# Optimization experiments

Hardware: AMD Instinct MI355X
Metric: run time of the kernel (lower is better)

The kernel has to match this reference:

```python
import jax, jax.numpy as jnp
import numpy as np

N_NODES = 50000
N_EDGES = 800000
IN_NF = 64
OUT_NF = 64
HID = 128
H = 4
D = 64
HD = H * D
EDGE_IN = 2 * IN_NF + 1 + 6   # 135
MSG_IN = HID + 1 + 3 + 6      # 138


def _p(key, i, shape, scale=0.02):
    return scale * jax.random.normal(jax.random.fold_in(key, i), shape, dtype=jnp.float32)


def setup_inputs() -> dict:
    key = jax.random.key(0)
    ks = jax.random.split(key, 4)
    inp = {
        "h": jax.random.normal(ks[0], (N_NODES, IN_NF), dtype=jnp.float32),
        "x": jax.random.normal(ks[1], (N_NODES, 3), dtype=jnp.float32),
        "edge_index": jax.random.randint(ks[2], (2, N_EDGES), 0, N_NODES, dtype=jnp.int32),
        "mask": jnp.ones((N_EDGES,), dtype=bool),
    }
    pk = jax.random.fold_in(key, 7)
    i = iter(range(100))
    inp.update({
        "Wq": _p(pk, next(i), (IN_NF, HD)), "bq": jnp.zeros((HD,)),
        "Wk": _p(pk, next(i), (IN_NF, HD)), "bk": jnp.zeros((HD,)),
        "Wv": _p(pk, next(i), (IN_NF, HD)), "bv": jnp.zeros((HD,)),
        "Wo": _p(pk, next(i), (HD, OUT_NF)), "bo": jnp.zeros((OUT_NF,)),
        "pw1": _p(pk, next(i), (1, HID // 2)), "pb1": jnp.zeros((HID // 2,)),
        "pw2": _p(pk, next(i), (HID // 2, H)), "pb2": jnp.zeros((H,)),
        "ew1": _p(pk, next(i), (EDGE_IN, HID)), "eb1": jnp.zeros((HID,)),
        "ew2": _p(pk, next(i), (HID, HID)), "eb2": jnp.zeros((HID,)),
        "eww": _p(pk, next(i), (HID, H)), "ewb": jnp.zeros((H,)),
        "mw1": _p(pk, next(i), (MSG_IN, HID)), "mb1": jnp.zeros((HID,)),
        "mw2": _p(pk, next(i), (HID, HID)), "mb2": jnp.zeros((HID,)),
        "gw": _p(pk, next(i), (HID, H)), "gb": jnp.zeros((H,)),
        "cw1": _p(pk, next(i), (HID, HID)), "cb1": jnp.zeros((HID,)),
        "cw2": _p(pk, next(i), (HID, H)), "cb2": jnp.zeros((H,)),
        "coord_weights": jnp.ones((H,)),
        "xw1": _p(pk, next(i), (HID, HID)), "xb1": jnp.zeros((HID,)),
        "xw2": _p(pk, next(i), (HID, H)), "xb2": jnp.zeros((H,)),
    })
    return inp


def reference(h, x, edge_index, mask,
              Wq, bq, Wk, bk, Wv, bv, Wo, bo,
              pw1, pb1, pw2, pb2,
              ew1, eb1, ew2, eb2, eww, ewb,
              mw1, mb1, mw2, mb2,
              gw, gb, cw1, cb1, cw2, cb2,
              coord_weights, xw1, xb1, xw2, xb2):
    silu = jax.nn.silu
    row, col = edge_index[0], edge_index[1]
    n = h.shape[0]

    q = (h @ Wq + bq).reshape(n, H, D)
    k = (h @ Wk + bk).reshape(n, H, D)
    v = (h @ Wv + bv).reshape(n, H, D)

    rel_pos = x[row] - x[col]                         # [E,3]
    rel_dist = jnp.sum(rel_pos ** 2, -1, keepdims=True)  # [E,1]
    pos_enc = silu(rel_dist @ pw1 + pb1) @ pw2 + pb2     # [E,H]

    # torch .std() is unbiased (ddof=1)
    xn = (x - x.mean(0, keepdims=True)) / (jnp.std(x, 0, keepdims=True, ddof=1) + 1e-8)

    edge_attr = jnp.concatenate([h[row], h[col], rel_dist, xn[row], xn[col]], -1)
    ef = silu(edge_attr @ ew1 + eb1) @ ew2 + eb2      # [E,HID]
    ewt = ef @ eww + ewb                              # [E,H]

    attn = jnp.einsum('ehd,ehd->eh', q[row], k[col]) / jnp.sqrt(jnp.float32(D))
    attn = attn + pos_enc + ewt
    attn = jnp.where(mask[:, None], attn, jnp.float32(-1e9))

    amax = jax.ops.segment_max(attn, row, num_segments=n)   # [N,H]
    attn = jnp.exp(attn - amax[row])
    asum = jax.ops.segment_sum(attn, row, num_segments=n)
    attn = attn / (asum[row] + 1e-8)                         # [E,H]

    msg_in = jnp.concatenate([ef, attn.mean(1, keepdims=True), rel_pos, xn[row], xn[col]], -1)
    msgs = silu(msg_in @ mw1 + mb1) @ mw2 + mb2              # [E,HID]

    gates = jax.nn.sigmoid(msgs @ gw + gb)                   # [E,H]
    cwts = silu(msgs @ cw1 + cb1) @ cw2 + cb2                # [E,H]

    # per-head index_add into the same buffer == sum over heads of the scalar weight
    s = jnp.sum(gates * cwts * coord_weights, -1, keepdims=True)  # [E,1]
    base = 0.9 * rel_pos + 0.1 * x[col]
    coord_update = jax.ops.segment_sum(s * base / (n - 1), row, num_segments=n)

    cross_v = jnp.cross(rel_pos, jnp.roll(rel_pos, 1, axis=0))
    cg = silu(msgs @ xw1 + xb1) @ xw2 + xb2                  # [E,H]
    cross_s = jnp.sum(cg, -1, keepdims=True)
    coord_update = coord_update + jax.ops.segment_sum(cross_s * cross_v / (n - 1), row, num_segments=n)

    wv = jax.ops.segment_sum(attn[..., None] * v[col], row, num_segments=n)  # [N,H,D]
    out = wv.reshape(n, HD) @ Wo + bo
    return out, coord_update
```

## Files before the change

kernel.cpp:

```cpp
#include <hip/hip_runtime.h>
#include <hip/hip_bf16.h>

#define NN 50000
#define NE 800000

typedef __bf16 bf16x8 __attribute__((ext_vector_type(8)));
typedef float f4v __attribute__((ext_vector_type(4)));

__device__ __forceinline__ float silu_f(float v){
  return v*__builtin_amdgcn_rcpf(1.0f+__expf(-v));
}
__device__ __forceinline__ float bf2f(unsigned int u){ return __uint_as_float(u<<16); }
__device__ __forceinline__ unsigned bfr(float f){
  unsigned b = __float_as_uint(f);
  return b + 0x7fffu + ((b>>16)&1u);
}
__device__ __forceinline__ unsigned short f2bf(float f){ return (unsigned short)(bfr(f)>>16); }
__device__ __forceinline__ unsigned pk2(float a, float b){
  unsigned r;
  asm("v_cvt_pk_bf16_f32 %0, %1, %2" : "=v"(r) : "v"(a), "v"(b));
  return r;
}

union U8 { unsigned short us[8]; uint4 u4; };

__device__ __forceinline__ void pack8(unsigned short* dst, float4 a, float4 b){
  uint4 u;
  u.x = pk2(a.x,a.y); u.y = pk2(a.z,a.w);
  u.z = pk2(b.x,b.y); u.w = pk2(b.z,b.w);
  *(uint4*)dst = u;
}

__device__ __forceinline__ int lidx(int e, int c, int CH){
  return (e*CH + ((c & ~7) | ((c ^ e) & 7))) << 3;
}

template<int KC, int CH>
__device__ __forceinline__ void gemm_rm(const unsigned short* act, const unsigned short* wf,
                                        int wu, int lane, f4v (&acc)[4][2]){
  int le = lane & 15, quad = lane >> 4;
  #pragma unroll
  for (int kc=0;kc<KC;kc++){
    bf16x8 a0 = *(const bf16x8*)(wf + (((wu*2  )*KC + kc)<<9) + lane*8);
    bf16x8 a1 = *(const bf16x8*)(wf + (((wu*2+1)*KC + kc)<<9) + lane*8);
    int chunk = kc*4 + quad;
    #pragma unroll
    for (int et=0;et<4;et++){
      bf16x8 b = *(const bf16x8*)(act + lidx(et*16+le, chunk, CH));
      acc[et][0] = __builtin_amdgcn_mfma_f32_16x16x32_bf16(a0, b, acc[et][0], 0,0,0);
      acc[et][1] = __builtin_amdgcn_mfma_f32_16x16x32_bf16(a1, b, acc[et][1], 0,0,0);
    }
  }
}

template<int CH, bool SILU, bool BIAS>
__device__ __forceinline__ void epi_rm(unsigned short* dst, const f4v (&acc)[4][2],
                                       const float* bias, int wu, int lane){
  int le = lane & 15, quad = lane >> 4;
  #pragma unroll
  for (int ot=0; ot<2; ot++){
    float4 bv = make_float4(0,0,0,0);
    if (BIAS) bv = *(const float4*)(bias + wu*32 + ot*16 + quad*4);
    int chunk = wu*4 + ot*2 + (quad>>1);
    int soff = (quad&1)*4;
    #pragma unroll
    for (int et=0; et<4; et++){
      float v0=acc[et][ot][0], v1=acc[et][ot][1], v2=acc[et][ot][2], v3=acc[et][ot][3];
      if (BIAS){ v0+=bv.x; v1+=bv.y; v2+=bv.z; v3+=bv.w; }
      if (SILU){ v0=silu_f(v0); v1=silu_f(v1); v2=silu_f(v2); v3=silu_f(v3); }
      uint2 u; u.x = pk2(v0,v1); u.y = pk2(v2,v3);
      *(uint2*)(dst + lidx(et*16+le, chunk, CH) + soff) = u;
    }
  }
}

template<int CH>
__device__ __forceinline__ void mfma_head(const unsigned short* buf, const unsigned short* whf,
                                          int wu, int lane, float* dst ){
  int le = lane & 15, quad = lane >> 4;
  f4v hacc = {0.f,0.f,0.f,0.f};
  #pragma unroll
  for (int kc=0;kc<4;kc++){
    bf16x8 a = *(const bf16x8*)(whf + (kc<<9) + lane*8);
    bf16x8 b = *(const bf16x8*)(buf + lidx(wu*16+le, kc*4+quad, CH));
    hacc = __builtin_amdgcn_mfma_f32_16x16x32_bf16(a, b, hacc, 0,0,0);
  }
  if (quad==0){
    #pragma unroll
    for (int r=0;r<4;r++) dst[r*65 + wu*16 + le] = hacc[r];
  }
}

__global__ __launch_bounds__(256) void k_zero(float* __restrict__ p, int n){
  int i = blockIdx.x*256 + threadIdx.x;
  if (i < n) p[i] = 0.f;
}

__global__ __launch_bounds__(256) void k_wcomb(const float* __restrict__ ew2, const float* __restrict__ eww,
                                               const float* __restrict__ eb2, const float* __restrict__ ewb,
                                               const float* __restrict__ pb2,
                                               float* __restrict__ wcomb, float* __restrict__ stats){
  int t = threadIdx.x;
  #pragma unroll
  for (int o=t;o<512;o+=256){
    int i=o>>2, hh=o&3;
    float s=0.f;
    for (int j=0;j<128;j++) s += ew2[i*128+j]*eww[j*4+hh];
    wcomb[o]=s;
  }
  if (t<4){
    float s=0.f;
    for (int j=0;j<128;j++) s += eb2[j]*eww[j*4+t];
    stats[12+t] = s + ewb[t] + pb2[t];
  }
}

__global__ __launch_bounds__(256) void k_wfold(const float* __restrict__ A, const float* __restrict__ Bm,
                                               const float* __restrict__ abias, const float* __restrict__ b2,
                                               float* __restrict__ dstW, float* __restrict__ dstB){
  int idx = blockIdx.x*256 + threadIdx.x;
  if (idx >= 129*128) return;
  int i = idx>>7, n = idx&127;
  if (i<128){
    float s=0.f;
    for (int j=0;j<128;j++) s += A[i*128+j]*Bm[j*128+n];
    dstW[i*128+n]=s;
  } else {
    float s=b2[n];
    for (int j=0;j<128;j++) s += abias[j]*Bm[j*128+n];
    dstB[n]=s;
  }
}

__global__ __launch_bounds__(256) void k_wfoldm(const float* __restrict__ ew2, const float* __restrict__ mw1,
                                                const float* __restrict__ eb2, const float* __restrict__ mb1,
                                                float* __restrict__ dstW, float* __restrict__ dstB){
  int idx = blockIdx.x*256 + threadIdx.x;
  if (idx >= 139*128) return;
  int i = idx>>7, n = idx&127;
  if (i<128){
    float s=0.f;
    for (int j=0;j<128;j++) s += ew2[i*128+j]*mw1[j*128+n];
    dstW[i*128+n]=s;
  } else if (i<138){
    dstW[i*128+n] = mw1[i*128+n];
  } else {
    float s=mb1[n];
    for (int j=0;j<128;j++) s += eb2[j]*mw1[j*128+n];
    dstB[n]=s;
  }
}

__global__ __launch_bounds__(256) void k_wfoldg(const float* __restrict__ mw2, const float* __restrict__ gw,
                                                const float* __restrict__ mb2, const float* __restrict__ gb,
                                                float* __restrict__ dstW, float* __restrict__ dstB){
  int idx = blockIdx.x*256 + threadIdx.x;
  if (idx >= 129*4) return;
  int i = idx>>2, hh = idx&3;
  if (i<128){
    float s=0.f;
    for (int j=0;j<128;j++) s += mw2[i*128+j]*gw[j*4+hh];
    dstW[i*4+hh]=s;
  } else {
    float s=gb[hh];
    for (int j=0;j<128;j++) s += mb2[j]*gw[j*4+hh];
    dstB[hh]=s;
  }
}

__global__ __launch_bounds__(256) void k_wprep(const float* __restrict__ src, unsigned short* __restrict__ dst,
                                               int Kreal, int KC){
  int idx = blockIdx.x*256 + threadIdx.x;
  int tot = 8*KC*512;
  if (idx >= tot) return;
  int nt  = idx/(KC*512); int rem = idx%(KC*512);
  int kc  = rem>>9;       int r2  = rem&511;
  int lq  = r2>>3;        int j   = r2&7;
  int k   = kc*32 + (lq>>4)*8 + j;
  int n   = nt*16 + (lq&15);
  float v = (k < Kreal) ? src[k*128 + n] : 0.f;
  dst[idx] = f2bf(v);
}

__global__ __launch_bounds__(256) void k_wprepq(const float* __restrict__ src, unsigned short* __restrict__ dst){
  int idx = blockIdx.x*256 + threadIdx.x;
  if (idx >= 16384) return;
  int nt  = idx>>10;  int rem = idx&1023;
  int kc  = rem>>9;   int r2  = rem&511;
  int lq  = r2>>3;    int j   = r2&7;
  int k   = kc*32 + (lq>>4)*8 + j;
  int n   = nt*16 + (lq&15);
  dst[idx] = f2bf(src[k*256 + n]);
}

__global__ __launch_bounds__(256) void k_wprep4(const float* __restrict__ src, unsigned short* __restrict__ dst){
  int idx = blockIdx.x*256 + threadIdx.x;
  if (idx >= 2048) return;
  int kc = idx>>9; int r2 = idx&511; int lq = r2>>3; int j = r2&7;
  int k = kc*32 + (lq>>4)*8 + j;
  int n = lq&15;
  dst[idx] = f2bf((n<4) ? src[k*4+n] : 0.f);
}

__global__ __launch_bounds__(256) void k_stats(const float* __restrict__ x, float* __restrict__ stats){
  int i = blockIdx.x*256 + threadIdx.x;
  float v0=0.f,v1=0.f,v2=0.f;
  if (i < NN){ v0=x[i*3+0]; v1=x[i*3+1]; v2=x[i*3+2]; }
  float vals[6] = {v0,v1,v2,v0*v0,v1*v1,v2*v2};
  __shared__ float red[256];
  for (int c=0;c<6;c++){
    red[threadIdx.x]=vals[c];
    __syncthreads();
    for (int off=128; off>0; off>>=1){
      if (threadIdx.x < off) red[threadIdx.x] += red[threadIdx.x+off];
      __syncthreads();
    }
    if (threadIdx.x==0) atomicAdd(&stats[c], red[0]);
    __syncthreads();
  }
}

__global__ __launch_bounds__(64) void k_statsfin(float* __restrict__ stats){
  int t = threadIdx.x;
  if (t < 3){
    float s = stats[t], sq = stats[3+t];
    float mean = s/(float)NN;
    float var = (sq - s*s/(float)NN)/(float)(NN-1);
    float sd = sqrtf(var);
    stats[6+t] = mean;
    stats[9+t] = 1.0f/(sd + 1e-8f);
  }
}

__global__ __launch_bounds__(256) void k_qkv2(const float* __restrict__ h,
    const unsigned short* __restrict__ wqf,
    const float* __restrict__ bq, const float* __restrict__ bk, const float* __restrict__ bv,
    unsigned short* __restrict__ q, unsigned short* __restrict__ kk, unsigned short* __restrict__ v){
  __shared__ __align__(16) unsigned short hstage[64*8*8];
  int t = threadIdx.x; int lane = t & 63; int w = t >> 6;
  int wu = __builtin_amdgcn_readfirstlane(w);
  int r0 = blockIdx.x*64;
  {
    int row = r0 + lane;
    float4 a = make_float4(0,0,0,0), b2 = make_float4(0,0,0,0),
           c = make_float4(0,0,0,0), d2 = make_float4(0,0,0,0);
    if (row < NN){
      const float* hr = h + (size_t)row*64 + wu*16;
      a  = *(const float4*)(hr);    b2 = *(const float4*)(hr+4);
      c  = *(const float4*)(hr+8);  d2 = *(const float4*)(hr+12);
    }
    pack8(&hstage[lidx(lane, 2*wu,   8)], a, b2);
    pack8(&hstage[lidx(lane, 2*wu+1, 8)], c, d2);
  }
  __syncthreads();
  int le = lane & 15, quad = lane >> 4;
  #pragma unroll
  for (int ti=0; ti<12; ti++){
    int tt = ti*4 + wu;
    f4v acc[4];
    f4v z = {0.f,0.f,0.f,0.f};
    acc[0]=z; acc[1]=z; acc[2]=z; acc[3]=z;
    #pragma unroll
    for (int kc=0;kc<2;kc++){
      bf16x8 a = *(const bf16x8*)(wqf + ((tt*2 + kc)<<9) + lane*8);
      int chunk = kc*4 + quad;
      #pragma unroll
      for (int et=0;et<4;et++){
        bf16x8 b = *(const bf16x8*)(hstage + lidx(et*16+le, chunk, 8));
        acc[et] = __builtin_amdgcn_mfma_f32_16x16x32_bf16(a, b, acc[et], 0,0,0);
      }
    }
    int mat = tt>>4; int ct = tt&15;
    const float* bias = (mat==0)? bq : (mat==1)? bk : bv;
    unsigned short* outp = (mat==0)? q : (mat==1)? kk : v;
    float4 bv4 = *(const float4*)(bias + ct*16 + quad*4);
    int col = ct*16 + quad*4;
    #pragma unroll
    for (int et=0;et<4;et++){
      int row2 = r0 + et*16 + le;
      if (row2 < NN){
        float v0=acc[et][0]+bv4.x, v1=acc[et][1]+bv4.y, v2=acc[et][2]+bv4.z, v3=acc[et][3]+bv4.w;
        if (mat<2){
          uint2 u; u.x = pk2(v0,v1); u.y = pk2(v2,v3);
          *(uint2*)(outp + (size_t)row2*256 + col) = u;
        } else {
          int head = col>>6, dd = col&63;
          unsigned short* vp = outp + (size_t)row2*256 + (size_t)dd*4 + head;
          vp[0]  = f2bf(v0);
          vp[4]  = f2bf(v1);
          vp[8]  = f2bf(v2);
          vp[12] = f2bf(v3);
        }
      }
    }
  }
}

__global__ __launch_bounds__(256) void k_count(const int* __restrict__ ei, int* __restrict__ counts){
  int e = blockIdx.x*256 + threadIdx.x;
  if (e < NE) atomicAdd(&counts[ei[e]], 1);
}

__global__ __launch_bounds__(256) void k_scan(int* __restrict__ counts, int* __restrict__ offs){
  __shared__ int ps[256];
  int t = threadIdx.x;
  int base = t*196;
  int s = 0;
  for (int i=0;i<196;i++){ int idx = base+i; if (idx < NN) s += counts[idx]; }
  ps[t]=s; __syncthreads();
  for (int off=1; off<256; off<<=1){
    int vv = (t>=off)? ps[t-off] : 0;
    __syncthreads();
    ps[t]+=vv;
    __syncthreads();
  }
  int run = ps[t]-s;
  for (int i=0;i<196;i++){
    int idx = base+i;
    if (idx < NN){ int c = counts[idx]; offs[idx]=run; counts[idx]=run; run+=c; }
  }
  if (t==255) offs[NN]=run;
}

__global__ __launch_bounds__(256) void k_fill(const int* __restrict__ ei, int* __restrict__ cursor, int* __restrict__ elist){
  int e = blockIdx.x*256 + threadIdx.x;
  if (e < NE){
    int r = ei[e];
    int p = atomicAdd(&cursor[r],1);
    elist[p] = e;
  }
}

__global__ __launch_bounds__(256) void k_e1(
    const float* __restrict__ h, const float* __restrict__ x, const int* __restrict__ ei,
    const float* __restrict__ stats,
    const unsigned short* __restrict__ qb, const unsigned short* __restrict__ kb,
    const unsigned short* __restrict__ wfrag, const unsigned short* __restrict__ whfrag,
    const float* __restrict__ eb1,
    const float* __restrict__ pw1, const float* __restrict__ pb1,
    const float* __restrict__ pw2,
    float* __restrict__ asum, float* __restrict__ eattn){
  __shared__ __align__(16) unsigned short bufIn[64*24*8];
  __shared__ float logit_s[256];
  __shared__ float ewt2_s[4*65];
  __shared__ float pos_s[4*65];
  __shared__ float rd_s[64], xnr_s[192], xnc_s[192];
  __shared__ int row_s[64], col_s[64];
  int t = threadIdx.x; int lane = t & 63; int w = t >> 6;
  int wu = __builtin_amdgcn_readfirstlane(w);
  int ebase = blockIdx.x * 64;

  for (int i=t;i<260;i+=256) pos_s[i]=0.f;
  if (t < 64){
    int ge = ebase + t;
    int r = ei[ge], c = ei[NE+ge];
    row_s[t]=r; col_s[t]=c;
    float xr0=x[r*3],xr1=x[r*3+1],xr2=x[r*3+2];
    float xc0=x[c*3],xc1=x[c*3+1],xc2=x[c*3+2];
    float rp0=xr0-xc0, rp1=xr1-xc1, rp2=xr2-xc2;
    rd_s[t]=rp0*rp0+rp1*rp1+rp2*rp2;
    float m0=stats[6],m1=stats[7],m2=stats[8],s0=stats[9],s1=stats[10],s2=stats[11];
    xnr_s[t*3+0]=(xr0-m0)*s0; xnr_s[t*3+1]=(xr1-m1)*s1; xnr_s[t*3+2]=(xr2-m2)*s2;
    xnc_s[t*3+0]=(xc0-m0)*s0; xnc_s[t*3+1]=(xc1-m1)*s1; xnc_s[t*3+2]=(xc2-m2)*s2;
  }
  __syncthreads();

  for (int ii=0; ii<16; ii++){
    int e = wu*16+ii;
    int r = row_s[e], c = col_s[e];
    uint2 qu = *(const uint2*)(qb + (size_t)r*256 + lane*4);
    uint2 ku = *(const uint2*)(kb + (size_t)c*256 + lane*4);
    float d = bf2f(qu.x&0xffffu)*bf2f(ku.x&0xffffu)
            + bf2f(qu.x>>16)   *bf2f(ku.x>>16)
            + bf2f(qu.y&0xffffu)*bf2f(ku.y&0xffffu)
            + bf2f(qu.y>>16)   *bf2f(ku.y>>16);
    d += __shfl_xor(d,1,16); d += __shfl_xor(d,2,16);
    d += __shfl_xor(d,4,16); d += __shfl_xor(d,8,16);
    if ((lane&15)==0) logit_s[e*4 + (lane>>4)] = d*0.125f;
  }
  {
    int jb = wu*16;
    float rd = rd_s[lane];
    float p0=0,p1=0,p2=0,p3=0;
    for (int j=jb; j<jb+16; j++){
      float hp = rd*pw1[j] + pb1[j];
      float hs = silu_f(hp);
      const float4 w4 = *(const float4*)(pw2 + j*4);
      p0+=hs*w4.x; p1+=hs*w4.y; p2+=hs*w4.z; p3+=hs*w4.w;
    }
    atomicAdd(&pos_s[0*65+lane],p0);
    atomicAdd(&pos_s[1*65+lane],p1);
    atomicAdd(&pos_s[2*65+lane],p2);
    atomicAdd(&pos_s[3*65+lane],p3);
  }
  {
    const float* hr = h + (size_t)row_s[lane]*64 + wu*16;
    pack8(&bufIn[lidx(lane, 2*wu,   24)], *(const float4*)(hr),   *(const float4*)(hr+4));
    pack8(&bufIn[lidx(lane, 2*wu+1, 24)], *(const float4*)(hr+8), *(const float4*)(hr+12));
    const float* hc = h + (size_t)col_s[lane]*64 + wu*16;
    pack8(&bufIn[lidx(lane, 8+2*wu, 24)], *(const float4*)(hc),   *(const float4*)(hc+4));
    pack8(&bufIn[lidx(lane, 9+2*wu, 24)], *(const float4*)(hc+8), *(const float4*)(hc+12));
  }
  if (t < 64){
    pack8(&bufIn[lidx(t,16,24)],
          make_float4(rd_s[t], xnr_s[t*3+0], xnr_s[t*3+1], xnr_s[t*3+2]),
          make_float4(xnc_s[t*3+0], xnc_s[t*3+1], xnc_s[t*3+2], 0.f));
  }
  {
    uint4 z4 = make_uint4(0,0,0,0);
    int e = t&63, j = t>>6;
    if (j < 3) *(uint4*)&bufIn[lidx(e, 17+j, 24)] = z4;
  }
  __syncthreads();
  f4v acc[4][2];
  f4v z = {0.f,0.f,0.f,0.f};
  #pragma unroll
  for (int et=0;et<4;et++){ acc[et][0]=z; acc[et][1]=z; }
  gemm_rm<5,24>(bufIn, wfrag + 0, wu, lane, acc);
  __syncthreads();
  epi_rm<24,true,true>(bufIn, acc, eb1, wu, lane);
  __syncthreads();
  mfma_head<24>(bufIn, whfrag + 0, wu, lane, ewt2_s);
  __syncthreads();
  {
    int e2 = t>>2, hh = t&3;
    float lg = logit_s[t] + stats[12+hh] + ewt2_s[hh*65+e2] + pos_s[hh*65+e2];
    float ex = __expf(lg);
    eattn[(size_t)ebase*4 + t] = ex;
    atomicAdd(&asum[row_s[e2]*4 + hh], ex);
  }
}

__global__ __launch_bounds__(256) void k_e2(
    const float* __restrict__ h, const float* __restrict__ x, const int* __restrict__ ei,
    const float* __restrict__ stats,
    const float* __restrict__ asum, const float* __restrict__ eattn,
    const unsigned short* __restrict__ wfrag, const unsigned short* __restrict__ whfrag,
    const float* __restrict__ eb1, const float* __restrict__ fbias,
    const float* __restrict__ cb2, const float* __restrict__ coordw,
    const float* __restrict__ xb2,
    float* __restrict__ cvec){
  __shared__ __align__(16) unsigned short bufIn[64*24*8];
  __shared__ float am_s[64];
  __shared__ float g_s[4*65], c_s[4*65], xx_s[4*65];
  __shared__ float s_s[64], cs_s[64];
  __shared__ float rp_s[192], rd_s[64], xnr_s[192], xnc_s[192], xc_s[192];
  __shared__ int row_s[64], col_s[64];
  int t = threadIdx.x; int lane = t & 63; int w = t >> 6;
  int wu = __builtin_amdgcn_readfirstlane(w);
  int ebase = blockIdx.x * 64;

  if (t < 64){
    int ge = ebase + t;
    int r = ei[ge], c = ei[NE+ge];
    row_s[t]=r; col_s[t]=c;
    float xr0=x[r*3],xr1=x[r*3+1],xr2=x[r*3+2];
    float xc0=x[c*3],xc1=x[c*3+1],xc2=x[c*3+2];
    float rp0=xr0-xc0, rp1=xr1-xc1, rp2=xr2-xc2;
    rp_s[t*3+0]=rp0; rp_s[t*3+1]=rp1; rp_s[t*3+2]=rp2;
    rd_s[t]=rp0*rp0+rp1*rp1+rp2*rp2;
    xc_s[t*3+0]=xc0; xc_s[t*3+1]=xc1; xc_s[t*3+2]=xc2;
    float m0=stats[6],m1=stats[7],m2=stats[8],s0=stats[9],s1=stats[10],s2=stats[11];
    xnr_s[t*3+0]=(xr0-m0)*s0; xnr_s[t*3+1]=(xr1-m1)*s1; xnr_s[t*3+2]=(xr2-m2)*s2;
    xnc_s[t*3+0]=(xc0-m0)*s0; xnc_s[t*3+1]=(xc1-m1)*s1; xnc_s[t*3+2]=(xc2-m2)*s2;
  }
  __syncthreads();
  {
    int e2 = t>>2; int hh = t&3;
    float ex = eattn[(size_t)ebase*4 + t];
    float a = ex / (asum[row_s[e2]*4 + hh] + 1e-8f);
    a += __shfl_xor(a,1); a += __shfl_xor(a,2);
    if (hh==0) am_s[e2] = 0.25f*a;
  }
  {
    const float* hr = h + (size_t)row_s[lane]*64 + wu*16;
    pack8(&bufIn[lidx(lane, 2*wu,   24)], *(const float4*)(hr),   *(const float4*)(hr+4));
    pack8(&bufIn[lidx(lane, 2*wu+1, 24)], *(const float4*)(hr+8), *(const float4*)(hr+12));
    const float* hc = h + (size_t)col_s[lane]*64 + wu*16;
    pack8(&bufIn[lidx(lane, 8+2*wu, 24)], *(const float4*)(hc),   *(const float4*)(hc+4));
    pack8(&bufIn[lidx(lane, 9+2*wu, 24)], *(const float4*)(hc+8), *(const float4*)(hc+12));
  }
  if (t < 64){
    pack8(&bufIn[lidx(t,16,24)],
          make_float4(rd_s[t], xnr_s[t*3+0], xnr_s[t*3+1], xnr_s[t*3+2]),
          make_float4(xnc_s[t*3+0], xnc_s[t*3+1], xnc_s[t*3+2], 0.f));
  }
  {
    uint4 z4 = make_uint4(0,0,0,0);
    int e = t&63, j = t>>6;
    if (j < 3) *(uint4*)&bufIn[lidx(e, 17+j, 24)] = z4;
  }
  __syncthreads();
  f4v acc[4][2];
  f4v z = {0.f,0.f,0.f,0.f};
  #pragma unroll
  for (int et=0;et<4;et++){ acc[et][0]=z; acc[et][1]=z; }
  gemm_rm<5,24>(bufIn, wfrag + 0, wu, lane, acc);
  __syncthreads();
  epi_rm<24,true,true>(bufIn, acc, eb1, wu, lane);
  if (t < 64){
    pack8(&bufIn[lidx(t,16,24)],
          make_float4(am_s[t], rp_s[t*3+0], rp_s[t*3+1], rp_s[t*3+2]),
          make_float4(xnr_s[t*3+0], xnr_s[t*3+1], xnr_s[t*3+2], xnc_s[t*3+0]));
    pack8(&bufIn[lidx(t,17,24)],
          make_float4(xnc_s[t*3+1], xnc_s[t*3+2], 0.f, 0.f),
          make_float4(0.f,0.f,0.f,0.f));
  }
  __syncthreads();
  #pragma unroll
  for (int et=0;et<4;et++){ acc[et][0]=z; acc[et][1]=z; }
  gemm_rm<5,24>(bufIn, wfrag + 20480, wu, lane, acc);
  __syncthreads();
  epi_rm<24,true,true>(bufIn, acc, fbias + 0, wu, lane);
  __syncthreads();
  mfma_head<24>(bufIn, whfrag + 2048, wu, lane, g_s);
  f4v ax[4][2];
  #pragma unroll
  for (int et=0;et<4;et++){ acc[et][0]=z; acc[et][1]=z; ax[et][0]=z; ax[et][1]=z; }
  {
    const unsigned short* wfc = wfrag + 40960;
    const unsigned short* wfx = wfrag + 57344;
    int le = lane&15, quad = lane>>4;
    #pragma unroll
    for (int kc=0;kc<4;kc++){
      bf16x8 ac0 = *(const bf16x8*)(wfc + (((wu*2  )*4 + kc)<<9) + lane*8);
      bf16x8 ac1 = *(const bf16x8*)(wfc + (((wu*2+1)*4 + kc)<<9) + lane*8);
      bf16x8 ax0 = *(const bf16x8*)(wfx + (((wu*2  )*4 + kc)<<9) + lane*8);
      bf16x8 ax1 = *(const bf16x8*)(wfx + (((wu*2+1)*4 + kc)<<9) + lane*8);
      int chunk = kc*4 + quad;
      #pragma unroll
      for (int et=0;et<4;et++){
        bf16x8 b = *(const bf16x8*)(bufIn + lidx(et*16+le, chunk, 24));
        acc[et][0] = __builtin_amdgcn_mfma_f32_16x16x32_bf16(ac0, b, acc[et][0], 0,0,0);
        acc[et][1] = __builtin_amdgcn_mfma_f32_16x16x32_bf16(ac1, b, acc[et][1], 0,0,0);
        ax[et][0]  = __builtin_amdgcn_mfma_f32_16x16x32_bf16(ax0, b, ax[et][0], 0,0,0);
        ax[et][1]  = __builtin_amdgcn_mfma_f32_16x16x32_bf16(ax1, b, ax[et][1], 0,0,0);
      }
    }
  }
  __syncthreads();
  epi_rm<24,true,true>(bufIn, acc, fbias + 128, wu, lane);
  __syncthreads();
  mfma_head<24>(bufIn, whfrag + 4096, wu, lane, c_s);
  __syncthreads();
  epi_rm<24,true,true>(bufIn, ax, fbias + 256, wu, lane);
  __syncthreads();
  mfma_head<24>(bufIn, whfrag + 6144, wu, lane, xx_s);
  __syncthreads();
  {
    int e2 = t>>2; int hh = t&3;
    float g = __builtin_amdgcn_rcpf(1.0f+__expf(-(g_s[hh*65+e2]+fbias[384+hh])));
    float cwv = c_s[hh*65+e2]+cb2[hh];
    float sv = g*cwv*coordw[hh];
    float csv = xx_s[hh*65+e2]+xb2[hh];
    sv += __shfl_xor(sv,1);  sv += __shfl_xor(sv,2);
    csv += __shfl_xor(csv,1); csv += __shfl_xor(csv,2);
    if (hh==0){ s_s[e2]=sv; cs_s[e2]=csv; }
  }
  __syncthreads();
  if (t < 64){
    int ge = ebase + t;
    float rp0=rp_s[t*3],rp1=rp_s[t*3+1],rp2=rp_s[t*3+2];
    float pp0,pp1,pp2;
    if (t > 0){ pp0=rp_s[(t-1)*3]; pp1=rp_s[(t-1)*3+1]; pp2=rp_s[(t-1)*3+2]; }
    else {
      int gp = (ebase==0)? (NE-1) : (ebase-1);
      int rr=ei[gp], cc2=ei[NE+gp];
      pp0=x[rr*3]-x[cc2*3]; pp1=x[rr*3+1]-x[cc2*3+1]; pp2=x[rr*3+2]-x[cc2*3+2];
    }
    float cv0 = rp1*pp2 - rp2*pp1;
    float cv1 = rp2*pp0 - rp0*pp2;
    float cv2 = rp0*pp1 - rp1*pp0;
    float sv = s_s[t], csv = cs_s[t];
    const float inv = 1.0f/49999.0f;
    cvec[(size_t)ge*3+0] = (sv*(0.9f*rp0+0.1f*xc_s[t*3+0]) + csv*cv0)*inv;
    cvec[(size_t)ge*3+1] = (sv*(0.9f*rp1+0.1f*xc_s[t*3+1]) + csv*cv1)*inv;
    cvec[(size_t)ge*3+2] = (sv*(0.9f*rp2+0.1f*xc_s[t*3+2]) + csv*cv2)*inv;
  }
}

__global__ __launch_bounds__(256) void k_aggout(
    const int* __restrict__ ei, const int* __restrict__ offs, const int* __restrict__ elist,
    const float* __restrict__ eattn, const unsigned short* __restrict__ vb,
    const float* __restrict__ cvec, const float* __restrict__ Wo, const float* __restrict__ bo,
    const float* __restrict__ asum,
    float* __restrict__ outp){
  __shared__ float wvs[4*256];
  int t = threadIdx.x; int lane = t & 63; int w = t >> 6;
  int node = blockIdx.x*4 + w;
  const int* colp = ei + NE;
  int s0 = offs[node], s1 = offs[node+1];
  float a0=0,a1=0,a2=0,a3=0,cc=0;
  int i = s0;
  for (; i+4<=s1; i+=4){
    int e0=elist[i], e1=elist[i+1], e2=elist[i+2], e3=elist[i+3];
    int c0=colp[e0], c1=colp[e1], c2=colp[e2], c3=colp[e3];
    uint2 v0 = *(const uint2*)(vb + (size_t)c0*256 + lane*4);
    uint2 v1 = *(const uint2*)(vb + (size_t)c1*256 + lane*4);
    uint2 v2 = *(const uint2*)(vb + (size_t)c2*256 + lane*4);
    uint2 v3 = *(const uint2*)(vb + (size_t)c3*256 + lane*4);
    float4 at0 = *(const float4*)(eattn + (size_t)e0*4);
    float4 at1 = *(const float4*)(eattn + (size_t)e1*4);
    float4 at2 = *(const float4*)(eattn + (size_t)e2*4);
    float4 at3 = *(const float4*)(eattn + (size_t)e3*4);
    if (lane < 3) cc += cvec[(size_t)e0*3+lane] + cvec[(size_t)e1*3+lane]
                      + cvec[(size_t)e2*3+lane] + cvec[(size_t)e3*3+lane];
    a0 += at0.x*bf2f(v0.x&0xffffu) + at1.x*bf2f(v1.x&0xffffu) + at2.x*bf2f(v2.x&0xffffu) + at3.x*bf2f(v3.x&0xffffu);
    a1 += at0.y*bf2f(v0.x>>16)     + at1.y*bf2f(v1.x>>16)     + at2.y*bf2f(v2.x>>16)     + at3.y*bf2f(v3.x>>16);
    a2 += at0.z*bf2f(v0.y&0xffffu) + at1.z*bf2f(v1.y&0xffffu) + at2.z*bf2f(v2.y&0xffffu) + at3.z*bf2f(v3.y&0xffffu);
    a3 += at0.w*bf2f(v0.y>>16)     + at1.w*bf2f(v1.y>>16)     + at2.w*bf2f(v2.y>>16)     + at3.w*bf2f(v3.y>>16);
  }
  for (; i<s1; i++){
    int e0 = elist[i];
    int c0 = colp[e0];
    uint2 v0 = *(const uint2*)(vb + (size_t)c0*256 + lane*4);
    float4 at0 = *(const float4*)(eattn + (size_t)e0*4);
    if (lane < 3) cc += cvec[(size_t)e0*3+lane];
    a0 += at0.x*bf2f(v0.x&0xffffu);
    a1 += at0.y*bf2f(v0.x>>16);
    a2 += at0.z*bf2f(v0.y&0xffffu);
    a3 += at0.w*bf2f(v0.y>>16);
  }
  {
    const float* as = asum + (size_t)node*4;
    a0 /= (as[0] + 1e-8f);
    a1 /= (as[1] + 1e-8f);
    a2 /= (as[2] + 1e-8f);
    a3 /= (as[3] + 1e-8f);
  }
  wvs[w*256 +       lane]=a0;
  wvs[w*256 +  64 + lane]=a1;
  wvs[w*256 + 128 + lane]=a2;
  wvs[w*256 + 192 + lane]=a3;
  if (lane < 3) outp[(size_t)NN*64 + (size_t)node*3 + lane] = cc;
  float o = bo[lane];
  #pragma unroll 4
  for (int k2=0;k2<256;k2++) o += wvs[w*256+k2] * Wo[k2*64+lane];
  outp[(size_t)node*64 + lane] = o;
}

extern "C" void kernel_launch(void* const* d_in, const int* in_sizes, int n_in,
                              void* d_out, int out_size, void* d_ws, size_t ws_size,
                              hipStream_t stream) {
  const float* h  = (const float*)d_in[0];
  const float* x  = (const float*)d_in[1];
  const int*   ei = (const int*)d_in[2];
  const float* Wq=(const float*)d_in[4];  const float* bq=(const float*)d_in[5];
  const float* Wk=(const float*)d_in[6];  const float* bk=(const float*)d_in[7];
  const float* Wv=(const float*)d_in[8];  const float* bv=(const float*)d_in[9];
  const float* Wo=(const float*)d_in[10]; const float* bo=(const float*)d_in[11];
  const float* pw1=(const float*)d_in[12]; const float* pb1=(const float*)d_in[13];
  const float* pw2=(const float*)d_in[14]; const float* pb2=(const float*)d_in[15];
  const float* ew1=(const float*)d_in[16]; const float* eb1=(const float*)d_in[17];
  const float* ew2=(const float*)d_in[18]; const float* eb2=(const float*)d_in[19];
  const float* eww=(const float*)d_in[20]; const float* ewb=(const float*)d_in[21];
  const float* mw1=(const float*)d_in[22]; const float* mb1=(const float*)d_in[23];
  const float* mw2=(const float*)d_in[24]; const float* mb2=(const float*)d_in[25];
  const float* gw=(const float*)d_in[26];  const float* gb=(const float*)d_in[27];
  const float* cw1=(const float*)d_in[28]; const float* cb1=(const float*)d_in[29];
  const float* cw2=(const float*)d_in[30]; const float* cb2=(const float*)d_in[31];
  const float* coordw=(const float*)d_in[32];
  const float* xw1=(const float*)d_in[33]; const float* xb1=(const float*)d_in[34];
  const float* xw2=(const float*)d_in[35]; const float* xb2=(const float*)d_in[36];

  char* B = (char*)d_ws;
  float* eattn = (float*)(B + 0);
  float* cvec  = (float*)(B + 12800000);
  float* stats = (float*)(B + 22400000);
  float* asum  = (float*)(B + 22400064);
  int* counts  = (int*)(B + 23200064);
  int* offs    = (int*)(B + 23400064);
  unsigned short* wfrag = (unsigned short*)(B + 23600080);
  int* elist   = (int*)(B + 23813088);
  unsigned short* qb = (unsigned short*)(B + 27013088);
  unsigned short* kb = (unsigned short*)(B + 52613088);
  unsigned short* vb = (unsigned short*)(B + 78213088);
  unsigned short* whfrag = (unsigned short*)(B + 103813088);
  float* fbias = (float*)(wfrag + 73728);
  float* wcomb = (float*)elist;
  float* wgf   = wcomb + 512;
  float* wmf   = wgf + 512;
  float* wcf   = wmf + 17664;
  float* wxf   = wcf + 16384;
  unsigned short* qkvf = (unsigned short*)eattn;

  k_zero<<<977,256,0,stream>>>(stats, 250016);
  k_wcomb<<<1,256,0,stream>>>(ew2, eww, eb2, ewb, pb2, wcomb, stats);
  k_wfoldm<<<70,256,0,stream>>>(ew2, mw1, eb2, mb1, wmf, fbias + 0);
  k_wfold<<<65,256,0,stream>>>(mw2, cw1, mb2, cb1, wcf, fbias + 128);
  k_wfold<<<65,256,0,stream>>>(mw2, xw1, mb2, xb1, wxf, fbias + 256);
  k_wfoldg<<<3,256,0,stream>>>(mw2, gw, mb2, gb, wgf, fbias + 384);
  k_wprep<<<80,256,0,stream>>>(ew1, wfrag + 0,     135, 5);
  k_wprep<<<80,256,0,stream>>>(wmf, wfrag + 20480, 138, 5);
  k_wprep<<<64,256,0,stream>>>(wcf, wfrag + 40960, 128, 4);
  k_wprep<<<64,256,0,stream>>>(wxf, wfrag + 57344, 128, 4);
  k_wprepq<<<64,256,0,stream>>>(Wq, qkvf + 0);
  k_wprepq<<<64,256,0,stream>>>(Wk, qkvf + 16384);
  k_wprepq<<<64,256,0,stream>>>(Wv, qkvf + 32768);
  k_wprep4<<<8,256,0,stream>>>(wcomb, whfrag + 0);
  k_wprep4<<<8,256,0,stream>>>(wgf, whfrag + 2048);
  k_wprep4<<<8,256,0,stream>>>(cw2, whfrag + 4096);
  k_wprep4<<<8,256,0,stream>>>(xw2, whfrag + 6144);

  k_stats<<<196,256,0,stream>>>(x, stats);
  k_statsfin<<<1,64,0,stream>>>(stats);
  k_qkv2<<<782,256,0,stream>>>(h, qkvf, bq, bk, bv, qb, kb, vb);
  k_count<<<3125,256,0,stream>>>(ei,counts);
  k_scan<<<1,256,0,stream>>>(counts,offs);
  k_fill<<<3125,256,0,stream>>>(ei,counts,elist);
  k_e1<<<12500,256,0,stream>>>(h,x,ei,stats,qb,kb,wfrag,whfrag,eb1,pw1,pb1,pw2,asum,eattn);
  k_e2<<<12500,256,0,stream>>>(h,x,ei,stats,asum,eattn,wfrag,whfrag,eb1,fbias,cb2,coordw,xb2,cvec);
  k_aggout<<<12500,256,0,stream>>>(ei,offs,elist,eattn,vb,cvec,Wo,bo,asum,(float*)d_out);
}
```

Baseline: 1.313 ms.

## Add second LDS activation buffer in k_e2 to drop barriers between GEMM stages

Adds a separate shared-memory buffer (bufA) for hidden activations so the first GEMM's epilogue can write without waiting for all waves to finish reading the input buffer. The message-side extra features are pre-packed into chunks 18-19 of the input buffer, and the folded message weight is re-laid out (zero-padded to 160 rows) so that its K chunk 4 reads those chunks directly. The coord and cross epilogues and heads now run back-to-back on two buffers, which removes several __syncthreads. The attention-mean computation moves into the per-edge packing thread. The cost is extra LDS per block, which may reduce occupancy.

```diff
diff --git a/kernel.cpp b/kernel.cpp
--- a/kernel.cpp
+++ b/kernel.cpp
@@ -136,14 +136,15 @@
                                                 const float* __restrict__ eb2, const float* __restrict__ mb1,
                                                 float* __restrict__ dstW, float* __restrict__ dstB){
   int idx = blockIdx.x*256 + threadIdx.x;
-  if (idx >= 139*128) return;
+  if (idx >= 161*128) return;
   int i = idx>>7, n = idx&127;
   if (i<128){
     float s=0.f;
     for (int j=0;j<128;j++) s += ew2[i*128+j]*mw1[j*128+n];
     dstW[i*128+n]=s;
-  } else if (i<138){
-    dstW[i*128+n] = mw1[i*128+n];
+  } else if (i<160){
+    int r = i-144;
+    dstW[i*128+n] = (r>=0 && r<10) ? mw1[(128+r)*128+n] : 0.f;
   } else {
     float s=mb1[n];
     for (int j=0;j<128;j++) s += eb2[j]*mw1[j*128+n];
@@ -441,7 +442,7 @@
     const float* __restrict__ xb2,
     float* __restrict__ cvec){
   __shared__ __align__(16) unsigned short bufIn[64*24*8];
-  __shared__ float am_s[64];
+  __shared__ __align__(16) unsigned short bufA [64*16*8];
   __shared__ float g_s[4*65], c_s[4*65], xx_s[4*65];
   __shared__ float s_s[64], cs_s[64];
   __shared__ float rp_s[192], rd_s[64], xnr_s[192], xnc_s[192], xc_s[192];
@@ -466,13 +467,6 @@
   }
   __syncthreads();
   {
-    int e2 = t>>2; int hh = t&3;
-    float ex = eattn[(size_t)ebase*4 + t];
-    float a = ex / (asum[row_s[e2]*4 + hh] + 1e-8f);
-    a += __shfl_xor(a,1); a += __shfl_xor(a,2);
-    if (hh==0) am_s[e2] = 0.25f*a;
-  }
-  {
     const float* hr = h + (size_t)row_s[lane]*64 + wu*16;
     pack8(&bufIn[lidx(lane, 2*wu,   24)], *(const float4*)(hr),   *(const float4*)(hr+4));
     pack8(&bufIn[lidx(lane, 2*wu+1, 24)], *(const float4*)(hr+8), *(const float4*)(hr+12));
@@ -481,14 +475,20 @@
     pack8(&bufIn[lidx(lane, 9+2*wu, 24)], *(const float4*)(hc+8), *(const float4*)(hc+12));
   }
   if (t < 64){
+    float4 at = *(const float4*)(eattn + (size_t)(ebase+t)*4);
+    const float* as4 = asum + (size_t)row_s[t]*4;
+    float am = 0.25f*( at.x/(as4[0]+1e-8f) + at.y/(as4[1]+1e-8f)
+                     + at.z/(as4[2]+1e-8f) + at.w/(as4[3]+1e-8f) );
     pack8(&bufIn[lidx(t,16,24)],
           make_float4(rd_s[t], xnr_s[t*3+0], xnr_s[t*3+1], xnr_s[t*3+2]),
           make_float4(xnc_s[t*3+0], xnc_s[t*3+1], xnc_s[t*3+2], 0.f));
-  }
-  {
-    uint4 z4 = make_uint4(0,0,0,0);
-    int e = t&63, j = t>>6;
-    if (j < 3) *(uint4*)&bufIn[lidx(e, 17+j, 24)] = z4;
+    *(uint4*)&bufIn[lidx(t,17,24)] = make_uint4(0,0,0,0);
+    pack8(&bufIn[lidx(t,18,24)],
+          make_float4(am, rp_s[t*3+0], rp_s[t*3+1], rp_s[t*3+2]),
+          make_float4(xnr_s[t*3+0], xnr_s[t*3+1], xnr_s[t*3+2], xnc_s[t*3+0]));
+    pack8(&bufIn[lidx(t,19,24)],
+          make_float4(xnc_s[t*3+1], xnc_s[t*3+2], 0.f, 0.f),
+          make_float4(0.f,0.f,0.f,0.f));
   }
   __syncthreads();
   f4v acc[4][2];
@@ -496,21 +496,27 @@
   #pragma unroll
   for (int et=0;et<4;et++){ acc[et][0]=z; acc[et][1]=z; }
   gemm_rm<5,24>(bufIn, wfrag + 0, wu, lane, acc);
-  __syncthreads();
-  epi_rm<24,true,true>(bufIn, acc, eb1, wu, lane);
-  if (t < 64){
-    pack8(&bufIn[lidx(t,16,24)],
-          make_float4(am_s[t], rp_s[t*3+0], rp_s[t*3+1], rp_s[t*3+2]),
-          make_float4(xnr_s[t*3+0], xnr_s[t*3+1], xnr_s[t*3+2], xnc_s[t*3+0]));
-    pack8(&bufIn[lidx(t,17,24)],
-          make_float4(xnc_s[t*3+1], xnc_s[t*3+2], 0.f, 0.f),
-          make_float4(0.f,0.f,0.f,0.f));
-  }
+  epi_rm<16,true,true>(bufA, acc, eb1, wu, lane);
   __syncthreads();
   #pragma unroll
   for (int et=0;et<4;et++){ acc[et][0]=z; acc[et][1]=z; }
-  gemm_rm<5,24>(bufIn, wfrag + 20480, wu, lane, acc);
-  __syncthreads();
+  {
+    const unsigned short* wf = wfrag + 20480;
+    int le = lane&15, quad = lane>>4;
+    #pragma unroll
+    for (int kc=0;kc<5;kc++){
+      bf16x8 a0 = *(const bf16x8*)(wf + (((wu*2  )*5 + kc)<<9) + lane*8);
+      bf16x8 a1 = *(const bf16x8*)(wf + (((wu*2+1)*5 + kc)<<9) + lane*8);
+      int chunk = kc*4 + quad;
+      #pragma unroll
+      for (int et=0;et<4;et++){
+        bf16x8 b = (kc<4) ? *(const bf16x8*)(bufA  + lidx(et*16+le, chunk, 16))
+                          : *(const bf16x8*)(bufIn + lidx(et*16+le, chunk, 24));
+        acc[et][0] = __builtin_amdgcn_mfma_f32_16x16x32_bf16(a0, b, acc[et][0], 0,0,0);
+        acc[et][1] = __builtin_amdgcn_mfma_f32_16x16x32_bf16(a1, b, acc[et][1], 0,0,0);
+      }
+    }
+  }
   epi_rm<24,true,true>(bufIn, acc, fbias + 0, wu, lane);
   __syncthreads();
   mfma_head<24>(bufIn, whfrag + 2048, wu, lane, g_s);
@@ -539,12 +545,10 @@
     }
   }
   __syncthreads();
-  epi_rm<24,true,true>(bufIn, acc, fbias + 128, wu, lane);
-  __syncthreads();
-  mfma_head<24>(bufIn, whfrag + 4096, wu, lane, c_s);
-  __syncthreads();
-  epi_rm<24,true,true>(bufIn, ax, fbias + 256, wu, lane);
-  __syncthreads();
+  epi_rm<16,true,true>(bufA,  acc, fbias + 128, wu, lane);
+  epi_rm<24,true,true>(bufIn, ax,  fbias + 256, wu, lane);
+  __syncthreads();
+  mfma_head<16>(bufA,  whfrag + 4096, wu, lane, c_s);
   mfma_head<24>(bufIn, whfrag + 6144, wu, lane, xx_s);
   __syncthreads();
   {
@@ -680,18 +684,18 @@
   float* wcomb = (float*)elist;
   float* wgf   = wcomb + 512;
   float* wmf   = wgf + 512;
-  float* wcf   = wmf + 17664;
+  float* wcf   = wmf + 20608;
   float* wxf   = wcf + 16384;
   unsigned short* qkvf = (unsigned short*)eattn;
 
   k_zero<<<977,256,0,stream>>>(stats, 250016);
   k_wcomb<<<1,256,0,stream>>>(ew2, eww, eb2, ewb, pb2, wcomb, stats);
-  k_wfoldm<<<70,256,0,stream>>>(ew2, mw1, eb2, mb1, wmf, fbias + 0);
+  k_wfoldm<<<81,256,0,stream>>>(ew2, mw1, eb2, mb1, wmf, fbias + 0);
   k_wfold<<<65,256,0,stream>>>(mw2, cw1, mb2, cb1, wcf, fbias + 128);
   k_wfold<<<65,256,0,stream>>>(mw2, xw1, mb2, xb1, wxf, fbias + 256);
   k_wfoldg<<<3,256,0,stream>>>(mw2, gw, mb2, gb, wgf, fbias + 384);
   k_wprep<<<80,256,0,stream>>>(ew1, wfrag + 0,     135, 5);
-  k_wprep<<<80,256,0,stream>>>(wmf, wfrag + 20480, 138, 5);
+  k_wprep<<<80,256,0,stream>>>(wmf, wfrag + 20480, 160, 5);
   k_wprep<<<64,256,0,stream>>>(wcf, wfrag + 40960, 128, 4);
   k_wprep<<<64,256,0,stream>>>(wxf, wfrag + 57344, 128, 4);
   k_wprepq<<<64,256,0,stream>>>(Wq, qkvf + 0);
```

New measurement: 1.290 ms. About the same (-1.8%).
